# Performance work log

Measured on AMD Instinct MI355X. Metric: run time of the kernel, lower is better.

## Reference

```python
import jax, jax.numpy as jnp
import numpy as np

B = 16
Dv, Hv, Wv = 128, 128, 128   # patchsize voxel grid (C=1)
NPTS = 1920                  # 16*120 points
EPS_IN = 1e-5                # InstanceNorm eps


def _inorm(x):
    # InstanceNorm1d, affine=False: normalize over last (length) dim per (b, c)
    m = jnp.mean(x, axis=-1, keepdims=True)
    v = jnp.var(x, axis=-1, keepdims=True)
    return (x - m) * jax.lax.rsqrt(v + EPS_IN)


def _mlp(q, w1, b1, w2, b2, w3, b3, w4, b4, w5, b5):
    b = q.shape[0]
    x = q.reshape(b, 256, 8)                                    # (b, 2048//8, 8)
    x = jnp.einsum('bil,oi->bol', x, w1) + b1[None, :, None]    # Conv1d(256,240,1) -> (b,240,8)
    x = jax.nn.relu(_inorm(x.reshape(b, 64, 30)))               # view (b,64,30), IN(64)
    # Conv1d(64,128,1,groups=64): each in-ch -> 2 out-chs; then view (b,32,120)
    x = (x[:, :, None, :] * w2[None, :, :, None] + b2.reshape(1, 64, 2, 1)).reshape(b, 32, 120)
    x = jax.nn.relu(_inorm(x))
    # Conv1d(32,64,1,groups=32); view (b,16,480)
    x = (x[:, :, None, :] * w3[None, :, :, None] + b3.reshape(1, 32, 2, 1)).reshape(b, 16, 480)
    x = jax.nn.relu(_inorm(x))
    # Conv1d(16,64,1,groups=16); view (b,16,1920)
    x = (x[:, :, None, :] * w4[None, :, :, None] + b4.reshape(1, 16, 4, 1)).reshape(b, 16, 1920)
    x = jax.nn.relu(_inorm(x))
    return jnp.einsum('bil,oi->bol', x, w5) + b5[None, :, None]  # Conv1d(16,3,1) -> (b,3,1920)


def _splat(vals, grid):
    # True adjoint of 3D grid_sample (align_corners=False, zeros padding):
    # trilinear scatter-add of point values into the voxel grid.
    # vals: (b, N); grid: (b, N, 3) with (x, y, z) ~ (W, H, D) normalized coords.
    b, n = vals.shape
    px = ((grid[..., 0] + 1.0) * Wv - 1.0) * 0.5
    py = ((grid[..., 1] + 1.0) * Hv - 1.0) * 0.5
    pz = ((grid[..., 2] + 1.0) * Dv - 1.0) * 0.5
    x0f = jnp.floor(px); y0f = jnp.floor(py); z0f = jnp.floor(pz)
    fx = px - x0f; fy = py - y0f; fz = pz - z0f
    x0 = x0f.astype(jnp.int32); y0 = y0f.astype(jnp.int32); z0 = z0f.astype(jnp.int32)
    bidx = jnp.arange(b, dtype=jnp.int32)[:, None]
    out = jnp.zeros(b * Dv * Hv * Wv, dtype=vals.dtype)
    for dz in (0, 1):
        wz = fz if dz else (1.0 - fz)
        for dy in (0, 1):
            wy = fy if dy else (1.0 - fy)
            for dx in (0, 1):
                wx = fx if dx else (1.0 - fx)
                xi = x0 + dx; yi = y0 + dy; zi = z0 + dz
                w = wx * wy * wz * vals
                valid = (xi >= 0) & (xi < Wv) & (yi >= 0) & (yi < Hv) & (zi >= 0) & (zi < Dv)
                w = jnp.where(valid, w, 0.0)
                xi = jnp.clip(xi, 0, Wv - 1)
                yi = jnp.clip(yi, 0, Hv - 1)
                zi = jnp.clip(zi, 0, Dv - 1)
                flat = ((bidx * Dv + zi) * Hv + yi) * Wv + xi
                out = out.at[flat.ravel()].add(w.ravel())
    return out.reshape(b, 1, Dv, Hv, Wv)


def _avgpool3(x):
    # AvgPool3d(3, stride=1, padding=1, count_include_pad=True) as separable 1D averages
    for ax in (2, 3, 4):
        pad = [(1, 1) if i == ax else (0, 0) for i in range(5)]
        xp = jnp.pad(x, pad)
        n = x.shape[ax]
        x = (jax.lax.slice_in_dim(xp, 0, n, axis=ax)
             + jax.lax.slice_in_dim(xp, 1, n + 1, axis=ax)
             + jax.lax.slice_in_dim(xp, 2, n + 2, axis=ax)) / 3.0
    return x


def _smooth(x):
    return _avgpool3(_avgpool3(_avgpool3(x)))


def _forward(q, q_val, w1, b1, w2, b2, w3, b3, w4, b4, w5, b5):
    b = q.shape[0]
    q3 = _mlp(q, w1, b1, w2, b2, w3, b3, w4, b4, w5, b5)   # (b, 3, 1920)
    coords = jnp.tanh(q3)                                    # q0_coord
    grid = jnp.transpose(coords, (0, 2, 1))                  # (b, 1920, 3)
    vals = jnp.broadcast_to(jax.nn.sigmoid(q_val).reshape(1, NPTS), (b, NPTS))
    out = _splat(vals, grid)
    out0 = _splat(jnp.ones((b, NPTS), q.dtype), grid)
    return _smooth(out) / (_smooth(out0) + 0.001)


def setup_inputs() -> dict:
    key = jax.random.key(0)
    ks = jax.random.split(key, 12)
    sc = 0.1
    return {
        'q': jax.random.normal(ks[0], (B, 2048), jnp.float32),
        'q_val': jax.random.normal(ks[1], (1, 1, 16, 120), jnp.float32),
        'w1': jax.random.normal(ks[2], (240, 256), jnp.float32) * sc,
        'b1': jax.random.normal(ks[3], (240,), jnp.float32) * sc,
        'w2': jax.random.normal(ks[4], (64, 2), jnp.float32) * sc,
        'b2': jax.random.normal(ks[5], (128,), jnp.float32) * sc,
        'w3': jax.random.normal(ks[6], (32, 2), jnp.float32) * sc,
        'b3': jax.random.normal(ks[7], (64,), jnp.float32) * sc,
        'w4': jax.random.normal(ks[8], (16, 4), jnp.float32) * sc,
        'b4': jax.random.normal(ks[9], (64,), jnp.float32) * sc,
        'w5': jax.random.normal(ks[10], (3, 16), jnp.float32) * sc,
        'b5': jax.random.normal(ks[11], (3,), jnp.float32) * sc,
    }


def reference(q, q_val, w1, b1, w2, b2, w3, b3, w4, b4, w5, b5):
    return _forward(q, q_val, w1, b1, w2, b2, w3, b3, w4, b4, w5, b5)
```

## Files before the change

kernel.cpp:

```cpp
#include <hip/hip_runtime.h>
#include <cstddef>

#define NB 16
#define NVOX 128
#define NPT 1920
#define NBINS 32768

static __device__ __forceinline__ float2 f2(float a, float b) {
    float2 r; r.x = a; r.y = b; return r;
}

__global__ __launch_bounds__(256)
void zero_out(float4* __restrict__ out)
{
    int idx = blockIdx.x * 2048 + threadIdx.x;
    #pragma unroll
    for (int i = 0; i < 8; ++i)
        out[idx + i * 256] = make_float4(0.f, 0.f, 0.f, 0.f);
}

__global__ __launch_bounds__(256)
void mlp_stage1(const float* __restrict__ q, const float* __restrict__ w1,
                const float* __restrict__ b1, float* __restrict__ x1g)
{
    __shared__ float wrow[256];
    __shared__ float psum[256];
    const int o = blockIdx.x;
    const int t = threadIdx.x;

    wrow[t] = w1[o * 256 + t];
    __syncthreads();

    const int half = t >> 7;
    const int bl = t & 127;
    const int b = bl >> 3, l = bl & 7;
    const float* qb = q + b * 2048 + l + half * 1024;
    float s = 0.f;
    #pragma unroll 8
    for (int i = 0; i < 128; ++i)
        s = fmaf(wrow[half * 128 + i], qb[i * 8], s);
    psum[t] = s;
    __syncthreads();

    if (t < 128) {
        int bb = t >> 3, ll = t & 7;
        x1g[bb * 1920 + o * 8 + ll] = b1[o] + psum[t] + psum[t + 128];
    }
}

__device__ __forceinline__ void bin_range(int x0, int y0, int z0,
                                          int& pxl, int& pxh, int& tyl, int& tyh,
                                          int& tzl, int& tzh)
{
    pxl = max(0, x0 - 3) >> 4; pxh = min(127, x0 + 4) >> 4;
    tyl = max(0, y0 - 3) >> 3; tyh = min(127, y0 + 4) >> 3;
    tzl = max(0, z0 - 3) >> 3; tzh = min(127, z0 + 4) >> 3;
}

__global__ __launch_bounds__(256)
void mlp_tail(const float* __restrict__ x1g, const float* __restrict__ qval,
              const float* __restrict__ w2, const float* __restrict__ b2,
              const float* __restrict__ w3, const float* __restrict__ b3,
              const float* __restrict__ w4, const float* __restrict__ b4,
              const float* __restrict__ w5, const float* __restrict__ b5,
              float4* __restrict__ pts)
{
    __shared__ float bufA[7680];
    __shared__ float bufC[3840];
    __shared__ float psum[256], psq[256];
    __shared__ float meanv[64], rstdv[64];
    __shared__ float m4[16], r4[16];

    const int b = blockIdx.x;
    const int t = threadIdx.x;

    for (int u = t; u < 1920; u += 256) bufA[u] = x1g[b * 1920 + u];
    __syncthreads();

    {
        int c = t >> 2, g = t & 3;
        float s = 0.f, s2 = 0.f;
        for (int p = g; p < 30; p += 4) { float v = bufA[c * 30 + p]; s += v; s2 += v * v; }
        psum[t] = s; psq[t] = s2;
    }
    __syncthreads();
    if (t < 64) {
        float s = 0.f, s2 = 0.f;
        for (int g = 0; g < 4; ++g) { s += psum[t * 4 + g]; s2 += psq[t * 4 + g]; }
        float m = s * (1.f / 30.f);
        float var = s2 * (1.f / 30.f) - m * m;
        meanv[t] = m; rstdv[t] = rsqrtf(var + 1e-5f);
    }
    __syncthreads();
    for (int k = t; k < 1920; k += 256) {
        int c = k / 30;
        bufA[k] = fmaxf((bufA[k] - meanv[c]) * rstdv[c], 0.f);
    }
    __syncthreads();

    for (int m = t; m < 3840; m += 256) {
        int c = m / 60;
        int r = m - c * 60;
        int j = r / 30;
        int p = r - j * 30;
        bufC[m] = fmaf(bufA[c * 30 + p], w2[c * 2 + j], b2[c * 2 + j]);
    }
    __syncthreads();
    {
        int c = t >> 3, g = t & 7;
        float s = 0.f, s2 = 0.f;
        for (int p = g; p < 120; p += 8) { float v = bufC[c * 120 + p]; s += v; s2 += v * v; }
        psum[t] = s; psq[t] = s2;
    }
    __syncthreads();
    if (t < 32) {
        float s = 0.f, s2 = 0.f;
        for (int g = 0; g < 8; ++g) { s += psum[t * 8 + g]; s2 += psq[t * 8 + g]; }
        float m = s * (1.f / 120.f);
        float var = s2 * (1.f / 120.f) - m * m;
        meanv[t] = m; rstdv[t] = rsqrtf(var + 1e-5f);
    }
    __syncthreads();
    for (int m = t; m < 3840; m += 256) {
        int c = m / 120;
        bufC[m] = fmaxf((bufC[m] - meanv[c]) * rstdv[c], 0.f);
    }
    __syncthreads();

    for (int m = t; m < 7680; m += 256) {
        int c = m / 240;
        int r = m - c * 240;
        int j = r / 120;
        int p = r - j * 120;
        bufA[m] = fmaf(bufC[c * 120 + p], w3[c * 2 + j], b3[c * 2 + j]);
    }
    __syncthreads();

    const int c3 = t >> 4, g3 = t & 15;
    {
        float s = 0.f, s2 = 0.f;
        for (int k = 0; k < 30; ++k) { float v = bufA[c3 * 480 + g3 + 16 * k]; s += v; s2 += v * v; }
        psum[t] = s; psq[t] = s2;
    }
    __syncthreads();
    if (t < 16) {
        float s = 0.f, s2 = 0.f;
        for (int g = 0; g < 16; ++g) { s += psum[t * 16 + g]; s2 += psq[t * 16 + g]; }
        float m = s * (1.f / 480.f);
        float var = s2 * (1.f / 480.f) - m * m;
        meanv[t] = m; rstdv[t] = rsqrtf(var + 1e-5f);
    }
    __syncthreads();
    {
        float m = meanv[c3], r = rstdv[c3];
        float s = 0.f, s2 = 0.f;
        for (int k = 0; k < 30; ++k) {
            int idx = c3 * 480 + g3 + 16 * k;
            float v = fmaxf((bufA[idx] - m) * r, 0.f);
            bufA[idx] = v; s += v; s2 += v * v;
        }
        psum[t] = s; psq[t] = s2;
    }
    __syncthreads();
    if (t < 16) {
        float s = 0.f, s2 = 0.f;
        for (int g = 0; g < 16; ++g) { s += psum[t * 16 + g]; s2 += psq[t * 16 + g]; }
        float sum4 = 0.f, sq4 = 0.f;
        for (int j = 0; j < 4; ++j) {
            float w = w4[t * 4 + j], bb = b4[t * 4 + j];
            sum4 += w * s + 480.f * bb;
            sq4  += w * w * s2 + 2.f * w * bb * s + 480.f * bb * bb;
        }
        float m = sum4 * (1.f / 1920.f);
        float var = sq4 * (1.f / 1920.f) - m * m;
        m4[t] = m; r4[t] = rsqrtf(var + 1e-5f);
    }
    __syncthreads();

    for (int l = t; l < NPT; l += 256) {
        int j = l / 480;
        int p = l - j * 480;
        float a0 = b5[0], a1 = b5[1], a2 = b5[2];
        #pragma unroll
        for (int c = 0; c < 16; ++c) {
            float xv = bufA[c * 480 + p];
            float x4 = fmaf(xv, w4[c * 4 + j], b4[c * 4 + j]);
            float h  = fmaxf((x4 - m4[c]) * r4[c], 0.f);
            a0 = fmaf(w5[c],      h, a0);
            a1 = fmaf(w5[16 + c], h, a1);
            a2 = fmaf(w5[32 + c], h, a2);
        }
        float px = tanhf(a0) * 64.f + 63.5f;
        float py = tanhf(a1) * 64.f + 63.5f;
        float pz = tanhf(a2) * 64.f + 63.5f;
        float val = 1.f / (1.f + expf(-qval[l]));
        float4 pv; pv.x = px; pv.y = py; pv.z = pz; pv.w = val;
        pts[b * NPT + l] = pv;
    }
}

__global__ __launch_bounds__(256)
void count_bins(const float4* __restrict__ pts, int* __restrict__ counts)
{
    __shared__ int hist[2048];
    const int b = blockIdx.x;
    const int t = threadIdx.x;
    for (int u = t; u < 2048; u += 256) hist[u] = 0;
    __syncthreads();

    for (int l = t; l < NPT; l += 256) {
        float4 pt = pts[b * NPT + l];
        int x0 = (int)floorf(pt.x), y0 = (int)floorf(pt.y), z0 = (int)floorf(pt.z);
        int pxl, pxh, tyl, tyh, tzl, tzh;
        bin_range(x0, y0, z0, pxl, pxh, tyl, tyh, tzl, tzh);
        for (int tz = tzl; tz <= tzh; ++tz)
            for (int ty = tyl; ty <= tyh; ++ty)
                for (int px_ = pxl; px_ <= pxh; ++px_)
                    atomicAdd(&hist[(tz * 16 + ty) * 8 + px_], 1);
    }
    __syncthreads();
    for (int u = t; u < 2048; u += 256) counts[b * 2048 + u] = hist[u];
}

__global__ __launch_bounds__(256)
void scan_a(const int* __restrict__ counts, int* __restrict__ offsets,
            int* __restrict__ part)
{
    __shared__ int sd[256];
    const int t = threadIdx.x;
    const int g = blockIdx.x * 256 + t;
    int v = counts[g];
    sd[t] = v;
    __syncthreads();
    for (int off = 1; off < 256; off <<= 1) {
        int u = (t >= off) ? sd[t - off] : 0;
        __syncthreads();
        sd[t] += u;
        __syncthreads();
    }
    offsets[g] = sd[t] - v;
    if (t == 255) part[blockIdx.x] = sd[t];
}

__global__ __launch_bounds__(128)
void scan_b(int* __restrict__ part, int* __restrict__ partoff,
            int* __restrict__ offsets)
{
    __shared__ int sd[128];
    const int t = threadIdx.x;
    int v = part[t];
    sd[t] = v;
    __syncthreads();
    for (int off = 1; off < 128; off <<= 1) {
        int u = (t >= off) ? sd[t - off] : 0;
        __syncthreads();
        sd[t] += u;
        __syncthreads();
    }
    partoff[t] = sd[t] - v;
    if (t == 127) offsets[NBINS] = sd[t];
}

__global__ __launch_bounds__(256)
void scan_c(int* __restrict__ offsets, const int* __restrict__ partoff,
            const int* __restrict__ counts, int* __restrict__ active,
            int* __restrict__ nact)
{
    const int g = blockIdx.x * 256 + threadIdx.x;
    offsets[g] += partoff[blockIdx.x];
    if (counts[g] != 0) {
        int p = atomicAdd(nact, 1);
        active[p] = g;
    }
}

__global__ __launch_bounds__(256)
void bin_fill(const float4* __restrict__ pts, const int* __restrict__ offsets,
              float4* __restrict__ binned)
{
    __shared__ int cur[2048];
    const int b = blockIdx.x;
    const int t = threadIdx.x;
    for (int u = t; u < 2048; u += 256) cur[u] = offsets[b * 2048 + u];
    __syncthreads();

    for (int l = t; l < NPT; l += 256) {
        float4 pt = pts[b * NPT + l];
        int x0 = (int)floorf(pt.x), y0 = (int)floorf(pt.y), z0 = (int)floorf(pt.z);
        int pxl, pxh, tyl, tyh, tzl, tzh;
        bin_range(x0, y0, z0, pxl, pxh, tyl, tyh, tzl, tzh);
        for (int tz = tzl; tz <= tzh; ++tz)
            for (int ty = tyl; ty <= tyh; ++ty)
                for (int px_ = pxl; px_ <= pxh; ++px_) {
                    int pos = atomicAdd(&cur[(tz * 16 + ty) * 8 + px_], 1);
                    binned[pos] = pt;
                }
    }
}

__device__ __forceinline__ void coef(int g, float& cm1, float& c0, float& cp1)
{
    cm1 = (g == 1 || g == 127) ? 5.f : 6.f;
    c0  = (g == 0 || g == 127) ? 4.f : 7.f;
    cp1 = (g == 0 || g == 126) ? 5.f : 6.f;
}

__global__ __launch_bounds__(256)
void tile_active(const float4* __restrict__ binned,
                 const int* __restrict__ offsets,
                 const int* __restrict__ active,
                 const int* __restrict__ nact,
                 float* __restrict__ out)
{
    __shared__ __align__(16) float2 raw[14 * 14 * 22];
    const int t = threadIdx.x;
    const int NA = *nact;

    for (int w = blockIdx.x; w < NA; w += gridDim.x) {
        const int code = active[w];
        const int pair = code & 7;
        const int ty   = (code >> 3) & 15;
        const int tz   = (code >> 7) & 15;
        const int b    = code >> 11;
        const int Tx = pair * 16, Ty = ty * 8, Tz = tz * 8;
        const int off = offsets[code];
        const int n   = offsets[code + 1] - off;
        float* ob = out + (((size_t)(b * NVOX + Tz) * NVOX + Ty) * NVOX + Tx);

        {
            float4* r4p = (float4*)raw;
            for (int u = t; u < 14 * 14 * 11; u += 256)
                r4p[u] = make_float4(0.f, 0.f, 0.f, 0.f);
        }
        __syncthreads();

        for (int p = t; p < n; p += 256) {
            float4 pt = binned[off + p];
            float x0f = floorf(pt.x), y0f = floorf(pt.y), z0f = floorf(pt.z);
            int x0 = (int)x0f, y0 = (int)y0f, z0 = (int)z0f;
            int lx0 = x0 - Tx + 3, ly0 = y0 - Ty + 3, lz0 = z0 - Tz + 3;
            float fx = pt.x - x0f, fy = pt.y - y0f, fz = pt.z - z0f;
            float val = pt.w;
            #pragma unroll
            for (int dz = 0; dz < 2; ++dz) {
                int zi = z0 + dz, lz = lz0 + dz;
                if ((unsigned)zi >= 128u || (unsigned)lz >= 14u) continue;
                float wz = dz ? fz : 1.f - fz;
                #pragma unroll
                for (int dy = 0; dy < 2; ++dy) {
                    int yi = y0 + dy, ly = ly0 + dy;
                    if ((unsigned)yi >= 128u || (unsigned)ly >= 14u) continue;
                    float wy = dy ? fy : 1.f - fy;
                    #pragma unroll
                    for (int dx = 0; dx < 2; ++dx) {
                        int xi = x0 + dx, lx = lx0 + dx;
                        if ((unsigned)xi >= 128u || (unsigned)lx >= 22u) continue;
                        float w = (dx ? fx : 1.f - fx) * wy * wz;
                        float2* cell = &raw[(lz * 14 + ly) * 22 + lx];
                        atomicAdd(&cell->x, w * val);
                        atomicAdd(&cell->y, w);
                    }
                }
            }
        }
        __syncthreads();

        for (int cc = t; cc < 14 * 22; cc += 256) {
            int ly = cc / 22, lx = cc - ly * 22;
            float2 v[14];
            #pragma unroll
            for (int j = 0; j < 14; ++j) v[j] = raw[(j * 14 + ly) * 22 + lx];
            #pragma unroll
            for (int k = 0; k < 8; ++k) {
                float cm1, c0, cp1; coef(Tz + k, cm1, c0, cp1);
                float sx = (v[k].x + v[k + 6].x) + 3.f * (v[k + 1].x + v[k + 5].x)
                         + cm1 * v[k + 2].x + c0 * v[k + 3].x + cp1 * v[k + 4].x;
                float sy = (v[k].y + v[k + 6].y) + 3.f * (v[k + 1].y + v[k + 5].y)
                         + cm1 * v[k + 2].y + c0 * v[k + 3].y + cp1 * v[k + 4].y;
                raw[((k + 3) * 14 + ly) * 22 + lx] = f2(sx * (1.f / 27.f), sy * (1.f / 27.f));
            }
        }
        __syncthreads();

        if (t < 8 * 22) {
            int lz = t / 22, lx = t - lz * 22;
            float2 v[14];
            #pragma unroll
            for (int j = 0; j < 14; ++j) v[j] = raw[((lz + 3) * 14 + j) * 22 + lx];
            #pragma unroll
            for (int k = 0; k < 8; ++k) {
                float cm1, c0, cp1; coef(Ty + k, cm1, c0, cp1);
                float sx = (v[k].x + v[k + 6].x) + 3.f * (v[k + 1].x + v[k + 5].x)
                         + cm1 * v[k + 2].x + c0 * v[k + 3].x + cp1 * v[k + 4].x;
                float sy = (v[k].y + v[k + 6].y) + 3.f * (v[k + 1].y + v[k + 5].y)
                         + cm1 * v[k + 2].y + c0 * v[k + 3].y + cp1 * v[k + 4].y;
                raw[((lz + 3) * 14 + (k + 3)) * 22 + lx] = f2(sx * (1.f / 27.f), sy * (1.f / 27.f));
            }
        }
        __syncthreads();

        {
            int row = t >> 2, qx = t & 3;
            int z = row >> 3, y = row & 7;
            const float2* base = &raw[((z + 3) * 14 + (y + 3)) * 22];
            float2 m[10];
            #pragma unroll
            for (int j = 0; j < 10; ++j) m[j] = base[4 * qx + j];
            float4 res;
            float* rp = (float*)&res;
            #pragma unroll
            for (int xi = 0; xi < 4; ++xi) {
                int gx = Tx + 4 * qx + xi;
                float cm1, c0, cp1; coef(gx, cm1, c0, cp1);
                float sx = (m[xi].x + m[xi + 6].x) + 3.f * (m[xi + 1].x + m[xi + 5].x)
                         + cm1 * m[xi + 2].x + c0 * m[xi + 3].x + cp1 * m[xi + 4].x;
                float sy = (m[xi].y + m[xi + 6].y) + 3.f * (m[xi + 1].y + m[xi + 5].y)
                         + cm1 * m[xi + 2].y + c0 * m[xi + 3].y + cp1 * m[xi + 4].y;
                rp[xi] = (sx * (1.f / 27.f)) / (sy * (1.f / 27.f) + 0.001f);
            }
            *(float4*)(ob + ((size_t)z * NVOX + y) * NVOX + qx * 4) = res;
        }
        __syncthreads();
    }
}

extern "C" void kernel_launch(void* const* d_in, const int* in_sizes, int n_in,
                              void* d_out, int out_size, void* d_ws, size_t ws_size,
                              hipStream_t stream)
{
    const float* q    = (const float*)d_in[0];
    const float* qval = (const float*)d_in[1];
    const float* w1   = (const float*)d_in[2];
    const float* b1   = (const float*)d_in[3];
    const float* w2   = (const float*)d_in[4];
    const float* b2   = (const float*)d_in[5];
    const float* w3   = (const float*)d_in[6];
    const float* b3   = (const float*)d_in[7];
    const float* w4   = (const float*)d_in[8];
    const float* b4   = (const float*)d_in[9];
    const float* w5   = (const float*)d_in[10];
    const float* b5   = (const float*)d_in[11];
    float* out = (float*)d_out;

    char* wsb = (char*)d_ws;
    int*    counts  = (int*)(wsb + 0x000000);
    int*    nact    = (int*)(wsb + 0x020000);
    int*    part    = (int*)(wsb + 0x020100);
    int*    partoff = (int*)(wsb + 0x020500);
    int*    offsets = (int*)(wsb + 0x020900);
    int*    active  = (int*)(wsb + 0x041000);
    float4* pts     = (float4*)(wsb + 0x061000);
    float4* binned  = (float4*)(wsb + 0x0D9000);
    float*  x1g     = (float*)(wsb + 0x500000);

    hipMemsetAsync(nact, 0, 4, stream);

    zero_out<<<4096, 256, 0, stream>>>((float4*)out);

    mlp_stage1<<<240, 256, 0, stream>>>(q, w1, b1, x1g);

    mlp_tail<<<NB, 256, 0, stream>>>(x1g, qval, w2, b2, w3, b3,
                                     w4, b4, w5, b5, pts);

    count_bins<<<NB, 256, 0, stream>>>(pts, counts);

    scan_a<<<128, 256, 0, stream>>>(counts, offsets, part);
    scan_b<<<1, 128, 0, stream>>>(part, partoff, offsets);
    scan_c<<<128, 256, 0, stream>>>(offsets, partoff, counts, active, nact);

    bin_fill<<<NB, 256, 0, stream>>>(pts, offsets, binned);

    tile_active<<<1024, 256, 0, stream>>>(binned, offsets, active, nact, out);
}
```

Measured before the change: 257.0 us.

## Gather smoothed splat per output tile directly, drop zero pass and active list

```diff
diff --git a/kernel.cpp b/kernel.cpp
--- a/kernel.cpp
+++ b/kernel.cpp
@@ -5,19 +5,7 @@
 #define NVOX 128
 #define NPT 1920
 #define NBINS 32768
-
-static __device__ __forceinline__ float2 f2(float a, float b) {
-    float2 r; r.x = a; r.y = b; return r;
-}
-
-__global__ __launch_bounds__(256)
-void zero_out(float4* __restrict__ out)
-{
-    int idx = blockIdx.x * 2048 + threadIdx.x;
-    #pragma unroll
-    for (int i = 0; i < 8; ++i)
-        out[idx + i * 256] = make_float4(0.f, 0.f, 0.f, 0.f);
-}
+#define CH 128
 
 __global__ __launch_bounds__(256)
 void mlp_stage1(const float* __restrict__ q, const float* __restrict__ w1,
@@ -49,10 +37,10 @@
 }
 
 __device__ __forceinline__ void bin_range(int x0, int y0, int z0,
-                                          int& pxl, int& pxh, int& tyl, int& tyh,
+                                          int& txl, int& txh, int& tyl, int& tyh,
                                           int& tzl, int& tzh)
 {
-    pxl = max(0, x0 - 3) >> 4; pxh = min(127, x0 + 4) >> 4;
+    txl = max(0, x0 - 3) >> 4; txh = min(127, x0 + 4) >> 4;
     tyl = max(0, y0 - 3) >> 3; tyh = min(127, y0 + 4) >> 3;
     tzl = max(0, z0 - 3) >> 3; tzh = min(127, z0 + 4) >> 3;
 }
@@ -63,17 +51,19 @@
               const float* __restrict__ w3, const float* __restrict__ b3,
               const float* __restrict__ w4, const float* __restrict__ b4,
               const float* __restrict__ w5, const float* __restrict__ b5,
-              float4* __restrict__ pts)
+              float4* __restrict__ pts, int* __restrict__ counts)
 {
     __shared__ float bufA[7680];
     __shared__ float bufC[3840];
     __shared__ float psum[256], psq[256];
     __shared__ float meanv[64], rstdv[64];
     __shared__ float m4[16], r4[16];
+    __shared__ int hist[2048];
 
     const int b = blockIdx.x;
     const int t = threadIdx.x;
 
+    for (int u = t; u < 2048; u += 256) hist[u] = 0;
     for (int u = t; u < 1920; u += 256) bufA[u] = x1g[b * 1920 + u];
     __syncthreads();
 
@@ -196,27 +186,14 @@
         float val = 1.f / (1.f + expf(-qval[l]));
         float4 pv; pv.x = px; pv.y = py; pv.z = pz; pv.w = val;
         pts[b * NPT + l] = pv;
-    }
-}
-
-__global__ __launch_bounds__(256)
-void count_bins(const float4* __restrict__ pts, int* __restrict__ counts)
-{
-    __shared__ int hist[2048];
-    const int b = blockIdx.x;
-    const int t = threadIdx.x;
-    for (int u = t; u < 2048; u += 256) hist[u] = 0;
-    __syncthreads();
-
-    for (int l = t; l < NPT; l += 256) {
-        float4 pt = pts[b * NPT + l];
-        int x0 = (int)floorf(pt.x), y0 = (int)floorf(pt.y), z0 = (int)floorf(pt.z);
-        int pxl, pxh, tyl, tyh, tzl, tzh;
-        bin_range(x0, y0, z0, pxl, pxh, tyl, tyh, tzl, tzh);
+
+        int x0 = (int)floorf(px), y0 = (int)floorf(py), z0 = (int)floorf(pz);
+        int txl, txh, tyl, tyh, tzl, tzh;
+        bin_range(x0, y0, z0, txl, txh, tyl, tyh, tzl, tzh);
         for (int tz = tzl; tz <= tzh; ++tz)
             for (int ty = tyl; ty <= tyh; ++ty)
-                for (int px_ = pxl; px_ <= pxh; ++px_)
-                    atomicAdd(&hist[(tz * 16 + ty) * 8 + px_], 1);
+                for (int tx = txl; tx <= txh; ++tx)
+                    atomicAdd(&hist[(tz * 16 + ty) * 8 + tx], 1);
     }
     __syncthreads();
     for (int u = t; u < 2048; u += 256) counts[b * 2048 + u] = hist[u];
@@ -262,16 +239,10 @@
 }
 
 __global__ __launch_bounds__(256)
-void scan_c(int* __restrict__ offsets, const int* __restrict__ partoff,
-            const int* __restrict__ counts, int* __restrict__ active,
-            int* __restrict__ nact)
+void scan_c(int* __restrict__ offsets, const int* __restrict__ partoff)
 {
     const int g = blockIdx.x * 256 + threadIdx.x;
     offsets[g] += partoff[blockIdx.x];
-    if (counts[g] != 0) {
-        int p = atomicAdd(nact, 1);
-        active[p] = g;
-    }
 }
 
 __global__ __launch_bounds__(256)
@@ -287,141 +258,104 @@
     for (int l = t; l < NPT; l += 256) {
         float4 pt = pts[b * NPT + l];
         int x0 = (int)floorf(pt.x), y0 = (int)floorf(pt.y), z0 = (int)floorf(pt.z);
-        int pxl, pxh, tyl, tyh, tzl, tzh;
-        bin_range(x0, y0, z0, pxl, pxh, tyl, tyh, tzl, tzh);
+        int txl, txh, tyl, tyh, tzl, tzh;
+        bin_range(x0, y0, z0, txl, txh, tyl, tyh, tzl, tzh);
         for (int tz = tzl; tz <= tzh; ++tz)
             for (int ty = tyl; ty <= tyh; ++ty)
-                for (int px_ = pxl; px_ <= pxh; ++px_) {
-                    int pos = atomicAdd(&cur[(tz * 16 + ty) * 8 + px_], 1);
+                for (int tx = txl; tx <= txh; ++tx) {
+                    int pos = atomicAdd(&cur[(tz * 16 + ty) * 8 + tx], 1);
                     binned[pos] = pt;
                 }
     }
 }
 
-__device__ __forceinline__ void coef(int g, float& cm1, float& c0, float& cp1)
-{
-    cm1 = (g == 1 || g == 127) ? 5.f : 6.f;
-    c0  = (g == 0 || g == 127) ? 4.f : 7.f;
-    cp1 = (g == 0 || g == 126) ? 5.f : 6.f;
-}
-
-__global__ __launch_bounds__(256)
-void tile_active(const float4* __restrict__ binned,
-                 const int* __restrict__ offsets,
-                 const int* __restrict__ active,
-                 const int* __restrict__ nact,
-                 float* __restrict__ out)
-{
-    __shared__ __align__(16) float2 raw[14 * 14 * 22];
-    const int t = threadIdx.x;
-    const int NA = *nact;
-
-    for (int w = blockIdx.x; w < NA; w += gridDim.x) {
-        const int code = active[w];
-        const int pair = code & 7;
-        const int ty   = (code >> 3) & 15;
-        const int tz   = (code >> 7) & 15;
-        const int b    = code >> 11;
-        const int Tx = pair * 16, Ty = ty * 8, Tz = tz * 8;
-        const int off = offsets[code];
-        const int n   = offsets[code + 1] - off;
-        float* ob = out + (((size_t)(b * NVOX + Tz) * NVOX + Ty) * NVOX + Tx);
-
-        {
-            float4* r4p = (float4*)raw;
-            for (int u = t; u < 14 * 14 * 11; u += 256)
-                r4p[u] = make_float4(0.f, 0.f, 0.f, 0.f);
-        }
-        __syncthreads();
-
-        for (int p = t; p < n; p += 256) {
-            float4 pt = binned[off + p];
+__device__ __forceinline__ float stap(int X, int d)
+{
+    int ad = d < 0 ? -d : d;
+    if (ad > 3) return 0.f;
+    if (ad == 3) return 1.f;
+    if (ad == 2) return 3.f;
+    if (d == -1) return (X == 1 || X == 127) ? 5.f : 6.f;
+    if (d == 0)  return (X == 0 || X == 127) ? 4.f : 7.f;
+    return (X == 0 || X == 126) ? 5.f : 6.f;
+}
+
+__device__ __forceinline__ void build_tab(float* tab, int c0, float f)
+{
+    const bool v0 = (c0 >= 0);
+    const bool v1 = (c0 + 1 <= 127);
+    #pragma unroll
+    for (int o = 0; o < 8; ++o) {
+        int X = c0 - 3 + o;
+        float v = 0.f;
+        if ((unsigned)X < 128u) {
+            if (v0) v += (1.f - f) * stap(X, 3 - o);
+            if (v1) v += f * stap(X, 4 - o);
+        }
+        tab[o] = v * (1.f / 27.f);
+    }
+}
+
+__global__ __launch_bounds__(256)
+void tile_out(const float4* __restrict__ binned, const int* __restrict__ offsets,
+              float* __restrict__ out)
+{
+    __shared__ float fxs[CH][8], fys[CH][8], fzs[CH][8];
+    __shared__ int   cxs[CH], cys[CH], czs[CH];
+    __shared__ float cvs[CH];
+
+    const int code = blockIdx.x;
+    const int tx   = code & 7;
+    const int ty   = (code >> 3) & 15;
+    const int tz   = (code >> 7) & 15;
+    const int b    = code >> 11;
+    const int Tx = tx * 16, Ty = ty * 8, Tz = tz * 8;
+    const int t = threadIdx.x;
+
+    const int off = offsets[code];
+    const int n   = offsets[code + 1] - off;
+
+    const int qx = t & 3, y = (t >> 2) & 7, z = t >> 5;
+    const int X0 = Tx + 4 * qx, Y = Ty + y, Z = Tz + z;
+
+    float num0 = 0.f, num1 = 0.f, num2 = 0.f, num3 = 0.f;
+    float den0 = 0.f, den1 = 0.f, den2 = 0.f, den3 = 0.f;
+
+    for (int base = 0; base < n; base += CH) {
+        const int chn = min(CH, n - base);
+        if (base) __syncthreads();
+        if (t < chn) {
+            float4 pt = binned[off + base + t];
             float x0f = floorf(pt.x), y0f = floorf(pt.y), z0f = floorf(pt.z);
             int x0 = (int)x0f, y0 = (int)y0f, z0 = (int)z0f;
-            int lx0 = x0 - Tx + 3, ly0 = y0 - Ty + 3, lz0 = z0 - Tz + 3;
-            float fx = pt.x - x0f, fy = pt.y - y0f, fz = pt.z - z0f;
-            float val = pt.w;
-            #pragma unroll
-            for (int dz = 0; dz < 2; ++dz) {
-                int zi = z0 + dz, lz = lz0 + dz;
-                if ((unsigned)zi >= 128u || (unsigned)lz >= 14u) continue;
-                float wz = dz ? fz : 1.f - fz;
-                #pragma unroll
-                for (int dy = 0; dy < 2; ++dy) {
-                    int yi = y0 + dy, ly = ly0 + dy;
-                    if ((unsigned)yi >= 128u || (unsigned)ly >= 14u) continue;
-                    float wy = dy ? fy : 1.f - fy;
-                    #pragma unroll
-                    for (int dx = 0; dx < 2; ++dx) {
-                        int xi = x0 + dx, lx = lx0 + dx;
-                        if ((unsigned)xi >= 128u || (unsigned)lx >= 22u) continue;
-                        float w = (dx ? fx : 1.f - fx) * wy * wz;
-                        float2* cell = &raw[(lz * 14 + ly) * 22 + lx];
-                        atomicAdd(&cell->x, w * val);
-                        atomicAdd(&cell->y, w);
-                    }
-                }
-            }
+            cxs[t] = x0; cys[t] = y0; czs[t] = z0; cvs[t] = pt.w;
+            build_tab(fxs[t], x0, pt.x - x0f);
+            build_tab(fys[t], y0, pt.y - y0f);
+            build_tab(fzs[t], z0, pt.z - z0f);
         }
         __syncthreads();
 
-        for (int cc = t; cc < 14 * 22; cc += 256) {
-            int ly = cc / 22, lx = cc - ly * 22;
-            float2 v[14];
-            #pragma unroll
-            for (int j = 0; j < 14; ++j) v[j] = raw[(j * 14 + ly) * 22 + lx];
-            #pragma unroll
-            for (int k = 0; k < 8; ++k) {
-                float cm1, c0, cp1; coef(Tz + k, cm1, c0, cp1);
-                float sx = (v[k].x + v[k + 6].x) + 3.f * (v[k + 1].x + v[k + 5].x)
-                         + cm1 * v[k + 2].x + c0 * v[k + 3].x + cp1 * v[k + 4].x;
-                float sy = (v[k].y + v[k + 6].y) + 3.f * (v[k + 1].y + v[k + 5].y)
-                         + cm1 * v[k + 2].y + c0 * v[k + 3].y + cp1 * v[k + 4].y;
-                raw[((k + 3) * 14 + ly) * 22 + lx] = f2(sx * (1.f / 27.f), sy * (1.f / 27.f));
-            }
-        }
-        __syncthreads();
-
-        if (t < 8 * 22) {
-            int lz = t / 22, lx = t - lz * 22;
-            float2 v[14];
-            #pragma unroll
-            for (int j = 0; j < 14; ++j) v[j] = raw[((lz + 3) * 14 + j) * 22 + lx];
-            #pragma unroll
-            for (int k = 0; k < 8; ++k) {
-                float cm1, c0, cp1; coef(Ty + k, cm1, c0, cp1);
-                float sx = (v[k].x + v[k + 6].x) + 3.f * (v[k + 1].x + v[k + 5].x)
-                         + cm1 * v[k + 2].x + c0 * v[k + 3].x + cp1 * v[k + 4].x;
-                float sy = (v[k].y + v[k + 6].y) + 3.f * (v[k + 1].y + v[k + 5].y)
-                         + cm1 * v[k + 2].y + c0 * v[k + 3].y + cp1 * v[k + 4].y;
-                raw[((lz + 3) * 14 + (k + 3)) * 22 + lx] = f2(sx * (1.f / 27.f), sy * (1.f / 27.f));
-            }
-        }
-        __syncthreads();
-
-        {
-            int row = t >> 2, qx = t & 3;
-            int z = row >> 3, y = row & 7;
-            const float2* base = &raw[((z + 3) * 14 + (y + 3)) * 22];
-            float2 m[10];
-            #pragma unroll
-            for (int j = 0; j < 10; ++j) m[j] = base[4 * qx + j];
-            float4 res;
-            float* rp = (float*)&res;
-            #pragma unroll
-            for (int xi = 0; xi < 4; ++xi) {
-                int gx = Tx + 4 * qx + xi;
-                float cm1, c0, cp1; coef(gx, cm1, c0, cp1);
-                float sx = (m[xi].x + m[xi + 6].x) + 3.f * (m[xi + 1].x + m[xi + 5].x)
-                         + cm1 * m[xi + 2].x + c0 * m[xi + 3].x + cp1 * m[xi + 4].x;
-                float sy = (m[xi].y + m[xi + 6].y) + 3.f * (m[xi + 1].y + m[xi + 5].y)
-                         + cm1 * m[xi + 2].y + c0 * m[xi + 3].y + cp1 * m[xi + 4].y;
-                rp[xi] = (sx * (1.f / 27.f)) / (sy * (1.f / 27.f) + 0.001f);
-            }
-            *(float4*)(ob + ((size_t)z * NVOX + y) * NVOX + qx * 4) = res;
-        }
-        __syncthreads();
-    }
+        for (int p = 0; p < chn; ++p) {
+            int oy = Y - cys[p] + 3;
+            int oz = Z - czs[p] + 3;
+            if ((oy | oz) & ~7) continue;
+            float fyz  = fys[p][oy] * fzs[p][oz];
+            float vfyz = cvs[p] * fyz;
+            int ox0 = X0 - cxs[p] + 3;
+            if ((unsigned)(ox0 + 0) < 8u) { float fv = fxs[p][ox0 + 0]; num0 = fmaf(vfyz, fv, num0); den0 = fmaf(fyz, fv, den0); }
+            if ((unsigned)(ox0 + 1) < 8u) { float fv = fxs[p][ox0 + 1]; num1 = fmaf(vfyz, fv, num1); den1 = fmaf(fyz, fv, den1); }
+            if ((unsigned)(ox0 + 2) < 8u) { float fv = fxs[p][ox0 + 2]; num2 = fmaf(vfyz, fv, num2); den2 = fmaf(fyz, fv, den2); }
+            if ((unsigned)(ox0 + 3) < 8u) { float fv = fxs[p][ox0 + 3]; num3 = fmaf(vfyz, fv, num3); den3 = fmaf(fyz, fv, den3); }
+        }
+    }
+
+    float4 res;
+    res.x = num0 / (den0 + 0.001f);
+    res.y = num1 / (den1 + 0.001f);
+    res.z = num2 / (den2 + 0.001f);
+    res.w = num3 / (den3 + 0.001f);
+    float* ob = out + (((size_t)(b * NVOX + Tz) * NVOX + Ty) * NVOX + Tx);
+    *(float4*)(ob + ((size_t)z * NVOX + y) * NVOX + qx * 4) = res;
 }
 
 extern "C" void kernel_launch(void* const* d_in, const int* in_sizes, int n_in,
@@ -444,31 +378,23 @@
 
     char* wsb = (char*)d_ws;
     int*    counts  = (int*)(wsb + 0x000000);
-    int*    nact    = (int*)(wsb + 0x020000);
-    int*    part    = (int*)(wsb + 0x020100);
-    int*    partoff = (int*)(wsb + 0x020500);
-    int*    offsets = (int*)(wsb + 0x020900);
-    int*    active  = (int*)(wsb + 0x041000);
-    float4* pts     = (float4*)(wsb + 0x061000);
-    float4* binned  = (float4*)(wsb + 0x0D9000);
-    float*  x1g     = (float*)(wsb + 0x500000);
-
-    hipMemsetAsync(nact, 0, 4, stream);
-
-    zero_out<<<4096, 256, 0, stream>>>((float4*)out);
+    int*    part    = (int*)(wsb + 0x020000);
+    int*    partoff = (int*)(wsb + 0x020400);
+    int*    offsets = (int*)(wsb + 0x020800);
+    float4* pts     = (float4*)(wsb + 0x041000);
+    float4* binned  = (float4*)(wsb + 0x0B9000);
+    float*  x1g     = (float*)(wsb + 0x480000);
 
     mlp_stage1<<<240, 256, 0, stream>>>(q, w1, b1, x1g);
 
     mlp_tail<<<NB, 256, 0, stream>>>(x1g, qval, w2, b2, w3, b3,
-                                     w4, b4, w5, b5, pts);
-
-    count_bins<<<NB, 256, 0, stream>>>(pts, counts);
+                                     w4, b4, w5, b5, pts, counts);
 
     scan_a<<<128, 256, 0, stream>>>(counts, offsets, part);
     scan_b<<<1, 128, 0, stream>>>(part, partoff, offsets);
-    scan_c<<<128, 256, 0, stream>>>(offsets, partoff, counts, active, nact);
+    scan_c<<<128, 256, 0, stream>>>(offsets, partoff);
 
     bin_fill<<<NB, 256, 0, stream>>>(pts, offsets, binned);
 
-    tile_active<<<1024, 256, 0, stream>>>(binned, offsets, active, nact, out);
-}
+    tile_out<<<NBINS, 256, 0, stream>>>(binned, offsets, out);
+}
```

Measured after the change: 413.0 us. 60.7% more time.
